# Optimization experiments

Hardware: AMD Instinct MI355X
Metric: run time of the kernel (lower is better)

## Reference

```python
import jax, jax.numpy as jnp
import numpy as np

NUM_ENT = 100000
NUM_REL = 500            # distinct relations; table holds 2*NUM_REL (forward + inverse)
E = 500000               # total edges: first half original, second half reversed
D = 200                  # init_dim = gcn_dim = embed_dim
B = 256
KW, KH = 10, 20          # ConvE reshape: 2*KW*KH == 2*D
NF, KS = 200, 7
FLAT = (2 * KW - KS + 1) * (KH - KS + 1) * NF  # 14*14*200 = 39200
EPS = 1e-5


def setup_inputs() -> dict:
    key = jax.random.key(0)
    k = jax.random.split(key, 24)
    half = E // 2
    src = jax.random.randint(k[0], (half,), 0, NUM_ENT)
    dst = jax.random.randint(k[1], (half,), 0, NUM_ENT)
    et = jax.random.randint(k[2], (half,), 0, NUM_REL)
    edge_index = jnp.stack([jnp.concatenate([src, dst]), jnp.concatenate([dst, src])])
    edge_type = jnp.concatenate([et, et + NUM_REL])
    sub = jax.random.randint(k[3], (B,), 0, NUM_ENT)
    rel = jax.random.randint(k[4], (B,), 0, 2 * NUM_REL)
    g = lambda i, shape, s=0.05: jax.random.normal(k[i], shape, jnp.float32) * s
    return dict(
        sub=sub, rel=rel, edge_index=edge_index, edge_type=edge_type,
        init_embed=g(5, (NUM_ENT, D)), init_rel=g(6, (2 * NUM_REL, D)),
        loop_rel1=g(7, (1, D)), loop_rel2=g(8, (1, D)),
        w_in1=g(9, (D, D)), w_out1=g(10, (D, D)), w_loop1=g(11, (D, D)), w_rel1=g(12, (D, D)), b1=jnp.zeros((D,), jnp.float32),
        w_in2=g(13, (D, D)), w_out2=g(14, (D, D)), w_loop2=g(15, (D, D)), w_rel2=g(16, (D, D)), b2=jnp.zeros((D,), jnp.float32),
        conv_w=g(17, (NF, 1, KS, KS)), conv_b=jnp.zeros((NF,), jnp.float32),
        bn0_g=jnp.ones((1,), jnp.float32), bn0_b=jnp.zeros((1,), jnp.float32),
        bn1_g=jnp.ones((NF,), jnp.float32), bn1_b=jnp.zeros((NF,), jnp.float32),
        bn2_g=jnp.ones((D,), jnp.float32), bn2_b=jnp.zeros((D,), jnp.float32),
        fc_w=g(18, (FLAT, D)), fc_b=jnp.zeros((D,), jnp.float32),
        ent_bias=jnp.zeros((NUM_ENT,), jnp.float32),
    )


def _bn2d(x, g, b):  # eval-mode BN: running mean 0, running var 1
    s = g / jnp.sqrt(1.0 + EPS)
    return x * s[None, :, None, None] + b[None, :, None, None]


def _bn1d(x, g, b):
    return x * (g / jnp.sqrt(1.0 + EPS)) + b


def _agg(x_src, rel_e, dst, w):
    # message = comp(h_src, h_rel) @ W   (subtraction composition), degree-normalized scatter
    m = (x_src - rel_e) @ w                                        # [E/2, D]
    s = jax.ops.segment_sum(m, dst, num_segments=NUM_ENT)          # [N, D]
    deg = jax.ops.segment_sum(jnp.ones(dst.shape, m.dtype), dst, num_segments=NUM_ENT)
    return s / jnp.clip(deg, 1.0)[:, None]


def _ragcn_layer(x, r, ei, et, w_in, w_out, w_loop, w_rel, loop_rel, b):
    half = ei.shape[1] // 2
    src, dst = ei[0], ei[1]
    re = r[et]                                                     # [E, D]
    res = (_agg(x[src[:half]], re[:half], dst[:half], w_in)
           + _agg(x[src[half:]], re[half:], dst[half:], w_out)
           + (x - loop_rel) @ w_loop)
    return jnp.tanh(res / 3.0 + b), r @ w_rel


def _forward(sub, rel, edge_index, edge_type, init_embed, init_rel,
             loop_rel1, loop_rel2, w_in1, w_out1, w_loop1, w_rel1, b1,
             w_in2, w_out2, w_loop2, w_rel2, b2, conv_w, conv_b,
             bn0_g, bn0_b, bn1_g, bn1_b, bn2_g, bn2_b, fc_w, fc_b, ent_bias):
    x, r = _ragcn_layer(init_embed, init_rel, edge_index, edge_type, w_in1, w_out1, w_loop1, w_rel1, loop_rel1, b1)
    x, r = _ragcn_layer(x, r, edge_index, edge_type, w_in2, w_out2, w_loop2, w_rel2, loop_rel2, b2)
    sub_emb = x[sub]                                               # [B, D]
    rel_emb = r[rel]                                               # [B, D]
    # ConvE concat: [B,2,D] -> [B,D,2] -> [B,1,2*KW,KH]
    stk = jnp.transpose(jnp.stack([sub_emb, rel_emb], axis=1), (0, 2, 1)).reshape(-1, 1, 2 * KW, KH)
    h = _bn2d(stk, bn0_g, bn0_b)
    h = jax.lax.conv_general_dilated(h, conv_w, (1, 1), 'VALID',
                                     dimension_numbers=('NCHW', 'OIHW', 'NCHW'))
    h = h + conv_b[None, :, None, None]
    h = jax.nn.relu(_bn2d(h, bn1_g, bn1_b))
    h = h.reshape(-1, FLAT)
    h = h @ fc_w + fc_b
    h = jax.nn.relu(_bn1d(h, bn2_g, bn2_b))
    logits = h @ x.T + ent_bias                                    # [B, NUM_ENT]
    return jax.nn.sigmoid(logits)


def reference(sub, rel, edge_index, edge_type, init_embed, init_rel,
              loop_rel1, loop_rel2, w_in1, w_out1, w_loop1, w_rel1, b1,
              w_in2, w_out2, w_loop2, w_rel2, b2, conv_w, conv_b,
              bn0_g, bn0_b, bn1_g, bn1_b, bn2_g, bn2_b, fc_w, fc_b, ent_bias):
    return _forward(sub, rel, edge_index, edge_type, init_embed, init_rel,
                    loop_rel1, loop_rel2, w_in1, w_out1, w_loop1, w_rel1, b1,
                    w_in2, w_out2, w_loop2, w_rel2, b2, conv_w, conv_b,
                    bn0_g, bn0_b, bn1_g, bn1_b, bn2_g, bn2_b, fc_w, fc_b, ent_bias)
```

## Files before the change

kernel.cpp:

```cpp
#include <hip/hip_runtime.h>
#include <math.h>

#define N_ENT   100000
#define N_REL2  1000
#define E_TOT   500000
#define E_HALF  250000
#define DIM     200
#define BB      256
#define NFILT   200
#define FLATK   39200
#define EPS_BN  1e-5f

#define NROWS   200000
#define SCHUNK  2048
#define SNBLK   ((NROWS + SCHUNK - 1) / SCHUNK)

#define FC_KC   175
#define FC_KLEN 224

typedef __attribute__((ext_vector_type(8))) short bf16x8;
typedef __attribute__((ext_vector_type(4))) float f32x4;

__device__ __forceinline__ unsigned short f2b(float f) {
    union { float f; unsigned u; } c; c.f = f;
    unsigned u = c.u;
    u += 0x7fffu + ((u >> 16) & 1u);
    return (unsigned short)(u >> 16);
}
__device__ __forceinline__ float b2f(unsigned short h) {
    union { unsigned u; float f; } c; c.u = ((unsigned)h) << 16;
    return c.f;
}
__device__ __forceinline__ float fast_tanh(float x) {
    float ax = fabsf(x);
    float e = __expf(-2.0f * ax);
    float t = (1.0f - e) / (1.0f + e);
    return copysignf(t, x);
}

__global__ void convert_kernel(const float* __restrict__ s, unsigned short* __restrict__ d,
                               int n) {
    int i = (blockIdx.x * 256 + threadIdx.x) * 4;
    if (i + 3 < n) {
        float4 v = *(const float4*)(s + i);
        ushort4 o;
        o.x = f2b(v.x); o.y = f2b(v.y); o.z = f2b(v.z); o.w = f2b(v.w);
        *(ushort4*)(d + i) = o;
    } else {
        for (; i < n; ++i) d[i] = f2b(s[i]);
    }
}

__global__ void wstack_kernel(const float* __restrict__ wIn, const float* __restrict__ wOut,
                              const float* __restrict__ wLoop, unsigned short* __restrict__ WTK) {
    int g = blockIdx.x * 256 + threadIdx.x;
    if (g >= 3 * 28 * 224 * 8) return;
    int kk = g & 7;
    int t = g >> 3;
    int col = t % 224;
    int t2 = t / 224;
    int unit = t2 % 28;
    int seg = t2 / 28;
    int k = unit * 8 + kk;
    float v = 0.f;
    if (col < 200 && k < 200)
        v = (seg == 0 ? wIn : seg == 1 ? wOut : wLoop)[k * 200 + col];
    WTK[g] = f2b(v);
}

__global__ void fwt_kernel(const float* __restrict__ fw, unsigned short* __restrict__ FWT) {
    __shared__ float t[32][33];
    const int bid = blockIdx.x;
    const int kt = bid % 1225, jt = bid / 1225;
    const int tid = threadIdx.x;
#pragma unroll
    for (int it = 0; it < 4; ++it) {
        int idx = tid + it * 256;
        int kk = idx >> 5, jj = idx & 31;
        int j = jt * 32 + jj;
        t[kk][jj] = (j < 200) ? fw[(size_t)(kt * 32 + kk) * 200 + j] : 0.f;
    }
    __syncthreads();
#pragma unroll
    for (int it = 0; it < 4; ++it) {
        int idx = tid + it * 256;
        int jj = idx >> 5, kk = idx & 31;
        int j = jt * 32 + jj;
        if (j < 208)
            FWT[(size_t)j * FLATK + kt * 32 + kk] = f2b(t[kk][jj]);
    }
}

__global__ void hist_kernel(const int* __restrict__ ei, int* __restrict__ cnt) {
    int e = blockIdx.x * 256 + threadIdx.x;
    if (e >= E_TOT) return;
    int row = ei[E_TOT + e] + (e < E_HALF ? 0 : N_ENT);
    atomicAdd(&cnt[row], 1);
}

__global__ void scan1_kernel(const int* __restrict__ cnt, int* __restrict__ row_start,
                             int* __restrict__ blockSum) {
    __shared__ int tsum[256];
    const int t = threadIdx.x;
    const int base = blockIdx.x * SCHUNK + t * 8;
    int v[8];
    int s = 0;
#pragma unroll
    for (int i = 0; i < 8; ++i) {
        int idx = base + i;
        int c = (idx < NROWS) ? cnt[idx] : 0;
        v[i] = s;
        s += c;
    }
    tsum[t] = s;
    __syncthreads();
    for (int off = 1; off < 256; off <<= 1) {
        int x = (t >= off) ? tsum[t - off] : 0;
        __syncthreads();
        if (t >= off) tsum[t] += x;
        __syncthreads();
    }
    int texc = (t == 0) ? 0 : tsum[t - 1];
    if (t == 0) blockSum[blockIdx.x] = tsum[255];
#pragma unroll
    for (int i = 0; i < 8; ++i) {
        int idx = base + i;
        if (idx < NROWS) row_start[idx] = texc + v[i];
    }
}

__global__ void scan2_kernel(int* __restrict__ blockSum) {
    int s = 0;
    for (int i = 0; i < SNBLK; ++i) { int c = blockSum[i]; blockSum[i] = s; s += c; }
}

__global__ void scan3_kernel(int* __restrict__ row_start, int* __restrict__ row_cur,
                             const int* __restrict__ blockSum) {
    int i = blockIdx.x * 256 + threadIdx.x;
    if (i >= NROWS) return;
    int v = row_start[i] + blockSum[i / SCHUNK];
    row_start[i] = v;
    row_cur[i] = v;
}

__global__ void fill_kernel(const int* __restrict__ ei, const int* __restrict__ et,
                            int* __restrict__ row_cur, int2* __restrict__ epair) {
    int e = blockIdx.x * 256 + threadIdx.x;
    if (e >= E_TOT) return;
    int row = ei[E_TOT + e] + (e < E_HALF ? 0 : N_ENT);
    int pos = atomicAdd(&row_cur[row], 1);
    epair[pos] = make_int2(ei[e], et[e]);
}

__global__ void gather_kernel(const unsigned short* __restrict__ x,
                              const unsigned short* __restrict__ r,
                              const int2* __restrict__ epair,
                              const int* __restrict__ row_start, const int* __restrict__ cnt,
                              unsigned short* __restrict__ agg) {
    int wid = blockIdx.x * 4 + (threadIdx.x >> 6);
    if (wid >= NROWS) return;
    int lane = threadIdx.x & 63;
    if (lane >= 50) return;
    int start = row_start[wid];
    int deg = cnt[wid];
    float a0 = 0.f, a1 = 0.f, a2 = 0.f, a3 = 0.f;
    float c0 = 0.f, c1 = 0.f, c2 = 0.f, c3 = 0.f;
    int i = 0;
    for (; i + 2 <= deg; i += 2) {
        int2 e0 = epair[start + i];
        int2 e1 = epair[start + i + 1];
        ushort4 xv0 = *(const ushort4*)(x + (size_t)e0.x * DIM + lane * 4);
        ushort4 rv0 = *(const ushort4*)(r + (size_t)e0.y * DIM + lane * 4);
        ushort4 xv1 = *(const ushort4*)(x + (size_t)e1.x * DIM + lane * 4);
        ushort4 rv1 = *(const ushort4*)(r + (size_t)e1.y * DIM + lane * 4);
        a0 += b2f(xv0.x) - b2f(rv0.x);
        a1 += b2f(xv0.y) - b2f(rv0.y);
        a2 += b2f(xv0.z) - b2f(rv0.z);
        a3 += b2f(xv0.w) - b2f(rv0.w);
        c0 += b2f(xv1.x) - b2f(rv1.x);
        c1 += b2f(xv1.y) - b2f(rv1.y);
        c2 += b2f(xv1.z) - b2f(rv1.z);
        c3 += b2f(xv1.w) - b2f(rv1.w);
    }
    if (i < deg) {
        int2 e = epair[start + i];
        ushort4 xv = *(const ushort4*)(x + (size_t)e.x * DIM + lane * 4);
        ushort4 rv = *(const ushort4*)(r + (size_t)e.y * DIM + lane * 4);
        a0 += b2f(xv.x) - b2f(rv.x);
        a1 += b2f(xv.y) - b2f(rv.y);
        a2 += b2f(xv.z) - b2f(rv.z);
        a3 += b2f(xv.w) - b2f(rv.w);
    }
    float sc = 1.0f / fmaxf((float)deg, 1.0f);
    ushort4 o;
    o.x = f2b((a0 + c0) * sc);
    o.y = f2b((a1 + c1) * sc);
    o.z = f2b((a2 + c2) * sc);
    o.w = f2b((a3 + c3) * sc);
    *(ushort4*)(agg + (size_t)wid * DIM + lane * 4) = o;
}

__global__ void lv_kernel(const float* __restrict__ lr, const float* __restrict__ wl,
                          float* __restrict__ lv) {
    int j = blockIdx.x * blockDim.x + threadIdx.x;
    if (j >= DIM) return;
    float acc = 0.f;
    for (int k = 0; k < DIM; ++k) acc += lr[k] * wl[k * DIM + j];
    lv[j] = acc;
}

__global__ void rgemm_kernel(const float* __restrict__ r, const float* __restrict__ w,
                             float* __restrict__ out, int rows) {
    int g = blockIdx.x * 256 + threadIdx.x;
    if (g >= rows * DIM) return;
    int i = g / DIM, j = g - i * DIM;
    float acc = 0.f;
    for (int k = 0; k < DIM; ++k) acc += r[i * DIM + k] * w[k * DIM + j];
    out[g] = acc;
}

#define LOAD_A1(g, slot) do {                                                   \
    const unsigned short* Ap_ = Aseg[(g) / 7];                                  \
    apf[slot] = *(const bf16x8*)(Ap_ + (size_t)arow * 200 + ((g) % 7) * 32 + lq * 8); \
} while (0)

__global__ __launch_bounds__(256, 5) void layer_mfma_kernel(
        const unsigned short* __restrict__ aggI, const unsigned short* __restrict__ aggO,
        const unsigned short* __restrict__ xin, const unsigned short* __restrict__ WTK,
        const float* __restrict__ lv, const float* __restrict__ bias,
        unsigned short* __restrict__ out, int nwg) {
    __shared__ unsigned short Wl[16 * 112 * 8];
    const int bid = blockIdx.x;
    const int q = nwg >> 3, rr = nwg & 7;
    const int xcd = bid & 7, idx = bid >> 3;
    const int L = (xcd < rr ? xcd * (q + 1) : rr * (q + 1) + (xcd - rr) * q) + idx;
    const int rowblk  = L >> 1;
    const int colbase = (L & 1) * 112;

    const int tid  = threadIdx.x;
    const int wm   = tid >> 6;
    const int lane = tid & 63;
    const int lr   = lane & 15;
    const int lq   = lane >> 4;
    const int row0 = rowblk * 64;
    const int arow = row0 + wm * 16 + lr;

    const unsigned short* const Aseg[3] = { aggI, aggO, xin };

    f32x4 acc[7];
#pragma unroll
    for (int n = 0; n < 7; ++n) acc[n] = (f32x4){0.f, 0.f, 0.f, 0.f};

    bf16x8 apf[4];
    LOAD_A1(0, 0);
    LOAD_A1(1, 1);
    LOAD_A1(2, 2);

#pragma unroll
    for (int seg = 0; seg < 3; ++seg) {
#pragma unroll
        for (int ph = 0; ph < 2; ++ph) {
            if (seg + ph) __syncthreads();
            if (ph == 0) {
#pragma unroll
                for (int it = 0; it < 7; ++it) {
                    int u = tid + it * 256;
                    int unit = u >> 7 , col;
                    unit = u / 112; col = u - unit * 112;
                    *(int4*)(&Wl[(unit * 112 + col) * 8]) =
                        *(const int4*)(WTK + ((size_t)(seg * 28 + unit) * 224 + colbase + col) * 8);
                }
            } else {
                for (int u = tid; u < 1344; u += 256) {
                    int unit = u / 112, col = u - unit * 112;
                    *(int4*)(&Wl[(unit * 112 + col) * 8]) =
                        *(const int4*)(WTK + ((size_t)(seg * 28 + 16 + unit) * 224 + colbase + col) * 8);
                }
            }
            __syncthreads();
            const int NC = (ph == 0) ? 4 : 3;
#pragma unroll
            for (int cc = 0; cc < NC; ++cc) {
                const int g = seg * 7 + (ph ? 4 : 0) + cc;
                if (g + 3 < 21) LOAD_A1(g + 3, (g + 3) & 3);
                __builtin_amdgcn_s_setprio(1);
#pragma unroll
                for (int n = 0; n < 7; ++n) {
                    bf16x8 b = *(const bf16x8*)(&Wl[((cc * 4 + lq) * 112 + n * 16 + lr) * 8]);
                    acc[n] = __builtin_amdgcn_mfma_f32_16x16x32_bf16(apf[g & 3], b, acc[n], 0, 0, 0);
                }
                __builtin_amdgcn_s_setprio(0);
            }
        }
    }

    {
        int rbase = row0 + wm * 16 + lq * 4;
#pragma unroll
        for (int n = 0; n < 7; ++n) {
            int col = colbase + n * 16 + lr;
            if (col < 200) {
                float lvc = lv[col], bc = bias[col];
#pragma unroll
                for (int r2 = 0; r2 < 4; ++r2) {
                    int row = rbase + r2;
                    if (row < N_ENT) {
                        float v = (acc[n][r2] - lvc) * (1.0f / 3.0f) + bc;
                        out[(size_t)row * 200 + col] = f2b(fast_tanh(v));
                    }
                }
            }
        }
    }
}

__global__ void img_kernel(const unsigned short* __restrict__ x, const float* __restrict__ r,
                           const int* __restrict__ sub, const int* __restrict__ rel,
                           const float* __restrict__ bn0g, const float* __restrict__ bn0b,
                           unsigned short* __restrict__ img) {
    int g = blockIdx.x * 256 + threadIdx.x;
    if (g >= BB * 2 * DIM) return;
    int b = g / 400, l = g - b * 400;
    int d = l >> 1;
    float v = (l & 1) ? r[(size_t)rel[b] * DIM + d] : b2f(x[(size_t)sub[b] * DIM + d]);
    float s0 = bn0g[0] * rsqrtf(1.0f + EPS_BN);
    img[g] = f2b(v * s0 + bn0b[0]);
}

__global__ void im2col_kernel(const unsigned short* __restrict__ img,
                              unsigned short* __restrict__ IM) {
    int g = blockIdx.x * 256 + threadIdx.x;
    if (g >= 50176 * 64) return;
    int row = g >> 6, k = g & 63;
    int b = row / 196, p = row - b * 196;
    int h = p / 14, w = p - h * 14;
    unsigned short v = 0;
    if (k < 49) {
        int i = k / 7, j = k - i * 7;
        v = img[b * 400 + (h + i) * 20 + (w + j)];
    }
    IM[g] = v;
}

__global__ void cwt_kernel(const float* __restrict__ cw, unsigned short* __restrict__ CWT) {
    int g = blockIdx.x * 256 + threadIdx.x;
    if (g >= 208 * 64) return;
    int f = g >> 6, k = g & 63;
    CWT[g] = (f < 200 && k < 49) ? f2b(cw[f * 49 + k]) : 0;
}

__global__ __launch_bounds__(256) void conv_mfma_kernel(
        const unsigned short* __restrict__ IM, const unsigned short* __restrict__ CWT,
        const float* __restrict__ cb, const float* __restrict__ bn1g,
        const float* __restrict__ bn1b, unsigned short* __restrict__ CO_B) {
    const int tid  = threadIdx.x;
    const int row0 = blockIdx.x * 128;
    const int wave = tid >> 6;
    const int lane = tid & 63;
    const int lr   = lane & 15;
    const int lq   = lane >> 4;
    const int arow = row0 + wave * 32 + lr;

    f32x4 acc[2][13];
#pragma unroll
    for (int m = 0; m < 2; ++m)
#pragma unroll
        for (int n = 0; n < 13; ++n) acc[m][n] = (f32x4){0.f, 0.f, 0.f, 0.f};

#pragma unroll
    for (int c = 0; c < 2; ++c) {
        const int k = c * 32 + lq * 8;
        bf16x8 a0 = *(const bf16x8*)(IM + (size_t)arow * 64 + k);
        bf16x8 a1 = *(const bf16x8*)(IM + (size_t)(arow + 16) * 64 + k);
#pragma unroll
        for (int n = 0; n < 13; ++n) {
            bf16x8 b = *(const bf16x8*)(CWT + (size_t)(n * 16 + lr) * 64 + k);
            acc[0][n] = __builtin_amdgcn_mfma_f32_16x16x32_bf16(a0, b, acc[0][n], 0, 0, 0);
            acc[1][n] = __builtin_amdgcn_mfma_f32_16x16x32_bf16(a1, b, acc[1][n], 0, 0, 0);
        }
    }

#pragma unroll
    for (int m = 0; m < 2; ++m) {
        int grow_base = row0 + wave * 32 + m * 16 + lq * 4;
#pragma unroll
        for (int n = 0; n < 13; ++n) {
            int col = n * 16 + lr;
            if (col < 200) {
                float s1 = bn1g[col] * rsqrtf(1.0f + EPS_BN);
                float t1 = bn1b[col];
                float cbf = cb[col];
#pragma unroll
                for (int r = 0; r < 4; ++r) {
                    int grow = grow_base + r;
                    int b = grow / 196, p = grow - b * 196;
                    float v = fmaxf((acc[m][n][r] + cbf) * s1 + t1, 0.f);
                    CO_B[(size_t)b * FLATK + col * 196 + p] = f2b(v);
                }
            }
        }
    }
}

__global__ __launch_bounds__(256) void fc_mfma_kernel(
        const unsigned short* __restrict__ CO_B, const unsigned short* __restrict__ FWT,
        float* __restrict__ partials) {
    const int tid  = threadIdx.x;
    const int kc   = blockIdx.x >> 2;
    const int mb   = blockIdx.x & 3;
    const int wave = tid >> 6;
    const int lane = tid & 63;
    const int lr   = lane & 15;
    const int lq   = lane >> 4;
    const int m0   = mb * 64 + wave * 16;

    f32x4 acc[13];
#pragma unroll
    for (int n = 0; n < 13; ++n) acc[n] = (f32x4){0.f, 0.f, 0.f, 0.f};

#pragma unroll
    for (int s = 0; s < 7; ++s) {
        const int k = kc * FC_KLEN + s * 32 + lq * 8;
        bf16x8 a = *(const bf16x8*)(CO_B + (size_t)(m0 + lr) * FLATK + k);
#pragma unroll
        for (int n = 0; n < 13; ++n) {
            bf16x8 b = *(const bf16x8*)(FWT + (size_t)(n * 16 + lr) * FLATK + k);
            acc[n] = __builtin_amdgcn_mfma_f32_16x16x32_bf16(a, b, acc[n], 0, 0, 0);
        }
    }

    float* slab = partials + (size_t)kc * (BB * 208);
#pragma unroll
    for (int n = 0; n < 13; ++n) {
        int col = n * 16 + lr;
#pragma unroll
        for (int r = 0; r < 4; ++r) {
            int row = m0 + lq * 4 + r;
            slab[(size_t)row * 208 + col] = acc[n][r];
        }
    }
}

__global__ void fc_reduce_kernel(const float* __restrict__ partials,
                                 const float* __restrict__ fcb,
                                 const float* __restrict__ g2, const float* __restrict__ b2v,
                                 unsigned short* __restrict__ hb) {
    int g = blockIdx.x * 256 + threadIdx.x;
    if (g >= BB * 224) return;
    int b = g / 224, j = g - b * 224;
    unsigned short o = 0;
    if (j < 200) {
        float s = 0.f;
        const float* p = partials + (size_t)b * 208 + j;
#pragma unroll 5
        for (int c = 0; c < FC_KC; ++c)
            s += p[(size_t)c * (BB * 208)];
        float v = (s + fcb[j]) * (g2[j] * rsqrtf(1.0f + EPS_BN)) + b2v[j];
        o = f2b(fmaxf(v, 0.f));
    }
    hb[g] = o;
}

#define LOAD_HB(g, buf) do {                                                    \
    const unsigned short* base_ = hb + (size_t)brow * 224 + (g) * 32 + lq * 8;  \
    buf[0] = *(const bf16x8*)(base_);                                           \
    buf[1] = *(const bf16x8*)(base_ + 16 * 224);                                \
} while (0)

__global__ __launch_bounds__(512, 2) void logits_mfma_kernel(
        const unsigned short* __restrict__ x, const unsigned short* __restrict__ hb,
        const float* __restrict__ eb, float* __restrict__ out, int nwg) {
    __shared__ unsigned short Xl[112 * 136];
    const int bid = blockIdx.x;
    const int q = nwg >> 3, rr = nwg & 7;
    const int xcd = bid & 7, idx = bid >> 3;
    const int nb = (xcd < rr ? xcd * (q + 1) : rr * (q + 1) + (xcd - rr) * q) + idx;
    const int ent0 = nb * 112;

    const int tid  = threadIdx.x;
    const int wave = tid >> 6;
    const int mh   = wave >> 2;
    const int wm   = wave & 3;
    const int lane = tid & 63;
    const int lr   = lane & 15;
    const int lq   = lane >> 4;
    const int brow = mh * 128 + wm * 32 + lr;

    f32x4 acc[2][7];
#pragma unroll
    for (int m = 0; m < 2; ++m)
#pragma unroll
        for (int n = 0; n < 7; ++n) acc[m][n] = (f32x4){0.f, 0.f, 0.f, 0.f};

    bf16x8 apf[3][2];
    LOAD_HB(0, apf[0]);
    LOAD_HB(1, apf[1]);

#pragma unroll
    for (int ph = 0; ph < 2; ++ph) {
        if (ph) __syncthreads();
        if (ph == 0) {
#pragma unroll
            for (int it = 0; it < 4; ++it) {
                int u = tid + it * 512;
                if (u < 1792) {
                    int row = u >> 4, c = u & 15;
                    int ent = ent0 + row;
                    int4 v = make_int4(0, 0, 0, 0);
                    if (ent < N_ENT)
                        v = *(const int4*)(x + (size_t)ent * 200 + c * 8);
                    *(int4*)(&Xl[row * 136 + c * 8]) = v;
                }
            }
        } else {
            for (int u = tid; u < 1344; u += 512) {
                int row = u / 12, c = u - row * 12;
                int gu = 16 + c;
                int ent = ent0 + row;
                int4 v = make_int4(0, 0, 0, 0);
                if (ent < N_ENT && gu < 25)
                    v = *(const int4*)(x + (size_t)ent * 200 + gu * 8);
                *(int4*)(&Xl[row * 136 + c * 8]) = v;
            }
        }
        __syncthreads();
        const int NC = (ph == 0) ? 4 : 3;
#pragma unroll
        for (int cc = 0; cc < NC; ++cc) {
            const int g = (ph ? 4 : 0) + cc;
            if (g + 2 < 7) LOAD_HB(g + 2, apf[(g + 2) % 3]);
#pragma unroll
            for (int n = 0; n < 7; ++n) {
                bf16x8 b = *(const bf16x8*)(&Xl[(n * 16 + lr) * 136 + cc * 32 + lq * 8]);
                acc[0][n] = __builtin_amdgcn_mfma_f32_16x16x32_bf16(apf[g % 3][0], b, acc[0][n], 0, 0, 0);
                acc[1][n] = __builtin_amdgcn_mfma_f32_16x16x32_bf16(apf[g % 3][1], b, acc[1][n], 0, 0, 0);
            }
        }
    }

#pragma unroll
    for (int m = 0; m < 2; ++m) {
        int b_base = mh * 128 + wm * 32 + m * 16 + lq * 4;
#pragma unroll
        for (int n = 0; n < 7; ++n) {
            int ent = ent0 + n * 16 + lr;
            if (ent < N_ENT) {
                float bias = eb[ent];
#pragma unroll
                for (int r = 0; r < 4; ++r) {
                    float v = acc[m][n][r] + bias;
                    out[(size_t)(b_base + r) * N_ENT + ent] = 1.0f / (1.0f + __expf(-v));
                }
            }
        }
    }
}

extern "C" void kernel_launch(void* const* d_in, const int* in_sizes, int n_in,
                              void* d_out, int out_size, void* d_ws, size_t ws_size,
                              hipStream_t stream) {
    const int*   sub        = (const int*)  d_in[0];
    const int*   rel        = (const int*)  d_in[1];
    const int*   edge_index = (const int*)  d_in[2];
    const int*   edge_type  = (const int*)  d_in[3];
    const float* init_embed = (const float*)d_in[4];
    const float* init_rel   = (const float*)d_in[5];
    const float* loop_rel1  = (const float*)d_in[6];
    const float* loop_rel2  = (const float*)d_in[7];
    const float* w_in1      = (const float*)d_in[8];
    const float* w_out1     = (const float*)d_in[9];
    const float* w_loop1    = (const float*)d_in[10];
    const float* w_rel1     = (const float*)d_in[11];
    const float* b1         = (const float*)d_in[12];
    const float* w_in2      = (const float*)d_in[13];
    const float* w_out2     = (const float*)d_in[14];
    const float* w_loop2    = (const float*)d_in[15];
    const float* w_rel2     = (const float*)d_in[16];
    const float* b2         = (const float*)d_in[17];
    const float* conv_w     = (const float*)d_in[18];
    const float* conv_b     = (const float*)d_in[19];
    const float* bn0_g      = (const float*)d_in[20];
    const float* bn0_b      = (const float*)d_in[21];
    const float* bn1_g      = (const float*)d_in[22];
    const float* bn1_b      = (const float*)d_in[23];
    const float* bn2_g      = (const float*)d_in[24];
    const float* bn2_b      = (const float*)d_in[25];
    const float* fc_w       = (const float*)d_in[26];
    const float* fc_b       = (const float*)d_in[27];
    const float* ent_bias   = (const float*)d_in[28];

    unsigned short* aggb = (unsigned short*)d_ws;
    unsigned short* x0b  = aggb + 40000000;
    unsigned short* x1b  = x0b  + 20000000;
    unsigned short* r0b  = x1b  + 20000000;
    unsigned short* r1b  = r0b  + 200000;
    unsigned short* WTK  = r1b  + 200000;
    unsigned short* img  = WTK  + 150528;
    unsigned short* IM   = img  + 102400;
    unsigned short* CWT  = IM   + 3211264;
    unsigned short* CO_B = CWT  + 13312;
    unsigned short* hb16 = CO_B + 10035200;
    unsigned short* FWT  = hb16 + 57344;
    float* fbase = (float*)(FWT + 8153600);
    float* r1f      = fbase;
    float* r2f      = r1f  + 200000;
    float* lv       = r2f  + 200000;
    float* partials = lv   + 256;

    int2* epair    = (int2*)CO_B;
    int* cnt       = (int*)(epair + E_TOT);
    int* row_start = cnt  + NROWS;
    int* row_cur   = row_start + NROWS;
    int* blockSum  = row_cur + NROWS;

    unsigned short* aggIb = aggb;
    unsigned short* aggOb = aggb + (size_t)N_ENT * DIM;
    unsigned short* x2b   = x0b;

    const int gather_blocks = (NROWS + 3) / 4;
    const int layer_nwg     = ((N_ENT + 63) / 64) * 2;
    const int logits_nwg    = (N_ENT + 111) / 112;
    const int wstack_blocks = (3 * 28 * 224 * 8 + 255) / 256;

    convert_kernel<<<(N_ENT * DIM + 1023) / 1024, 256, 0, stream>>>(init_embed, x0b, N_ENT * DIM);
    convert_kernel<<<(N_REL2 * DIM + 1023) / 1024, 256, 0, stream>>>(init_rel, r0b, N_REL2 * DIM);
    hipMemsetAsync(cnt, 0, (size_t)NROWS * 4, stream);
    hist_kernel<<<(E_TOT + 255) / 256, 256, 0, stream>>>(edge_index, cnt);
    scan1_kernel<<<SNBLK, 256, 0, stream>>>(cnt, row_start, blockSum);
    scan2_kernel<<<1, 1, 0, stream>>>(blockSum);
    scan3_kernel<<<(NROWS + 255) / 256, 256, 0, stream>>>(row_start, row_cur, blockSum);
    fill_kernel<<<(E_TOT + 255) / 256, 256, 0, stream>>>(edge_index, edge_type, row_cur, epair);

    wstack_kernel<<<wstack_blocks, 256, 0, stream>>>(w_in1, w_out1, w_loop1, WTK);
    gather_kernel<<<gather_blocks, 256, 0, stream>>>(x0b, r0b, epair, row_start, cnt, aggb);
    lv_kernel<<<1, 256, 0, stream>>>(loop_rel1, w_loop1, lv);
    layer_mfma_kernel<<<layer_nwg, 256, 0, stream>>>(aggIb, aggOb, x0b, WTK, lv, b1, x1b, layer_nwg);
    rgemm_kernel<<<(N_REL2 * DIM + 255) / 256, 256, 0, stream>>>(init_rel, w_rel1, r1f, N_REL2);
    convert_kernel<<<(N_REL2 * DIM + 1023) / 1024, 256, 0, stream>>>(r1f, r1b, N_REL2 * DIM);

    wstack_kernel<<<wstack_blocks, 256, 0, stream>>>(w_in2, w_out2, w_loop2, WTK);
    gather_kernel<<<gather_blocks, 256, 0, stream>>>(x1b, r1b, epair, row_start, cnt, aggb);
    lv_kernel<<<1, 256, 0, stream>>>(loop_rel2, w_loop2, lv);
    layer_mfma_kernel<<<layer_nwg, 256, 0, stream>>>(aggIb, aggOb, x1b, WTK, lv, b2, x2b, layer_nwg);
    rgemm_kernel<<<(N_REL2 * DIM + 255) / 256, 256, 0, stream>>>(r1f, w_rel2, r2f, N_REL2);

    img_kernel<<<(BB * 400 + 255) / 256, 256, 0, stream>>>(x2b, r2f, sub, rel,
                                                           bn0_g, bn0_b, img);
    im2col_kernel<<<(50176 * 64 + 255) / 256, 256, 0, stream>>>(img, IM);
    cwt_kernel<<<(208 * 64 + 255) / 256, 256, 0, stream>>>(conv_w, CWT);
    conv_mfma_kernel<<<50176 / 128, 256, 0, stream>>>(IM, CWT, conv_b, bn1_g, bn1_b, CO_B);
    fwt_kernel<<<1225 * 7, 256, 0, stream>>>(fc_w, FWT);
    fc_mfma_kernel<<<FC_KC * 4, 256, 0, stream>>>(CO_B, FWT, partials);
    fc_reduce_kernel<<<(BB * 224 + 255) / 256, 256, 0, stream>>>(partials, fc_b, bn2_g, bn2_b, hb16);

    logits_mfma_kernel<<<logits_nwg, 512, 0, stream>>>(x2b, hb16, ent_bias, (float*)d_out,
                                                       logits_nwg);
}
```

Baseline: 588.2 us.

## Double-buffer weight tiles in LDS with register prefetch in layer GEMM

Replaces the six-phase load-sync-compute loop for weight tiles with a double-buffered LDS scheme. Each stage holds two k-chunks, and the next stage is fetched into registers while MFMAs run on the current buffer. This is meant to hide global-load latency of the weight tiles behind compute and reduce exposed barrier stalls. In exchange there are more barriers (eleven stages), extra registers for staging, and launch bounds drop from 5 to 4 blocks per SM, which lowers occupancy.

```diff
diff --git a/kernel.cpp b/kernel.cpp
--- a/kernel.cpp
+++ b/kernel.cpp
@@ -224,12 +224,38 @@
     apf[slot] = *(const bf16x8*)(Ap_ + (size_t)arow * 200 + ((g) % 7) * 32 + lq * 8); \
 } while (0)
 
-__global__ __launch_bounds__(256, 5) void layer_mfma_kernel(
+#define STAGE_LOAD(s) do {                                                       \
+    _Pragma("unroll")                                                            \
+    for (int it = 0; it < 4; ++it) {                                             \
+        int u = tid + it * 256;                                                  \
+        if (u < 896) {                                                           \
+            int slot = u / 448;                                                  \
+            int rem  = u - slot * 448;                                           \
+            int ui   = rem / 112, col = rem - ui * 112;                          \
+            int g2   = (s) * 2 + slot;                                           \
+            if (g2 < 21) {                                                       \
+                int sg = g2 / 7, kc = g2 % 7;                                    \
+                vals[it] = *(const int4*)(WTK +                                  \
+                    ((size_t)(sg * 28 + kc * 4 + ui) * 224 + colbase + col) * 8);\
+            } else vals[it] = make_int4(0, 0, 0, 0);                             \
+        }                                                                        \
+    }                                                                            \
+} while (0)
+
+#define STAGE_WRITE(b) do {                                                      \
+    _Pragma("unroll")                                                            \
+    for (int it = 0; it < 4; ++it) {                                             \
+        int u = tid + it * 256;                                                  \
+        if (u < 896) *(int4*)(&Wl[(b)][u * 8]) = vals[it];                       \
+    }                                                                            \
+} while (0)
+
+__global__ __launch_bounds__(256, 4) void layer_mfma_kernel(
         const unsigned short* __restrict__ aggI, const unsigned short* __restrict__ aggO,
         const unsigned short* __restrict__ xin, const unsigned short* __restrict__ WTK,
         const float* __restrict__ lv, const float* __restrict__ bias,
         unsigned short* __restrict__ out, int nwg) {
-    __shared__ unsigned short Wl[16 * 112 * 8];
+    __shared__ unsigned short Wl[2][8 * 112 * 8];
     const int bid = blockIdx.x;
     const int q = nwg >> 3, rr = nwg & 7;
     const int xcd = bid & 7, idx = bid >> 3;
@@ -256,42 +282,30 @@
     LOAD_A1(1, 1);
     LOAD_A1(2, 2);
 
-#pragma unroll
-    for (int seg = 0; seg < 3; ++seg) {
-#pragma unroll
-        for (int ph = 0; ph < 2; ++ph) {
-            if (seg + ph) __syncthreads();
-            if (ph == 0) {
-#pragma unroll
-                for (int it = 0; it < 7; ++it) {
-                    int u = tid + it * 256;
-                    int unit = u >> 7 , col;
-                    unit = u / 112; col = u - unit * 112;
-                    *(int4*)(&Wl[(unit * 112 + col) * 8]) =
-                        *(const int4*)(WTK + ((size_t)(seg * 28 + unit) * 224 + colbase + col) * 8);
-                }
-            } else {
-                for (int u = tid; u < 1344; u += 256) {
-                    int unit = u / 112, col = u - unit * 112;
-                    *(int4*)(&Wl[(unit * 112 + col) * 8]) =
-                        *(const int4*)(WTK + ((size_t)(seg * 28 + 16 + unit) * 224 + colbase + col) * 8);
-                }
+    int4 vals[4];
+
+    STAGE_LOAD(0);
+    STAGE_WRITE(0);
+    __syncthreads();
+
+#pragma unroll
+    for (int p = 0; p < 11; ++p) {
+        if (p < 10) STAGE_LOAD(p + 1);
+        const int NC = (p < 10) ? 2 : 1;
+#pragma unroll
+        for (int cc = 0; cc < NC; ++cc) {
+            const int g = p * 2 + cc;
+            if (g + 3 < 21) LOAD_A1(g + 3, (g + 3) & 3);
+            __builtin_amdgcn_s_setprio(1);
+#pragma unroll
+            for (int n = 0; n < 7; ++n) {
+                bf16x8 b = *(const bf16x8*)(&Wl[p & 1][((cc * 4 + lq) * 112 + n * 16 + lr) * 8]);
+                acc[n] = __builtin_amdgcn_mfma_f32_16x16x32_bf16(apf[g & 3], b, acc[n], 0, 0, 0);
             }
-            __syncthreads();
-            const int NC = (ph == 0) ? 4 : 3;
-#pragma unroll
-            for (int cc = 0; cc < NC; ++cc) {
-                const int g = seg * 7 + (ph ? 4 : 0) + cc;
-                if (g + 3 < 21) LOAD_A1(g + 3, (g + 3) & 3);
-                __builtin_amdgcn_s_setprio(1);
-#pragma unroll
-                for (int n = 0; n < 7; ++n) {
-                    bf16x8 b = *(const bf16x8*)(&Wl[((cc * 4 + lq) * 112 + n * 16 + lr) * 8]);
-                    acc[n] = __builtin_amdgcn_mfma_f32_16x16x32_bf16(apf[g & 3], b, acc[n], 0, 0, 0);
-                }
-                __builtin_amdgcn_s_setprio(0);
-            }
-        }
+            __builtin_amdgcn_s_setprio(0);
+        }
+        if (p < 10) STAGE_WRITE((p + 1) & 1);
+        __syncthreads();
     }
 
     {
```

Result: faster. 569.2 us (median of 2 runs) (-3.2%).

## Switch layer GEMM to 32x32x16 MFMA with 128-row full-width tiles and double-buffered weights

Applied to the files above, without the earlier changes.

Reworks the per-layer MFMA kernel so each workgroup covers 128 rows and all 224 output columns, not 64 rows by half the columns. It uses 32x32x16 bf16 MFMA instructions and double-buffers the weight slices in LDS, prefetching the next stage into registers during compute. This removes duplicate A-row loads across the two column halves and overlaps weight staging with math. The cost is more accumulator registers and lower occupancy (launch bounds drop from 5 to 3 waves per SIMD), plus fewer workgroups overall.

```diff
diff --git a/kernel.cpp b/kernel.cpp
--- a/kernel.cpp
+++ b/kernel.cpp
@@ -20,6 +20,7 @@
 
 typedef __attribute__((ext_vector_type(8))) short bf16x8;
 typedef __attribute__((ext_vector_type(4))) float f32x4;
+typedef __attribute__((ext_vector_type(16))) float f32x16;
 
 __device__ __forceinline__ unsigned short f2b(float f) {
     union { float f; unsigned u; } c; c.f = f;
@@ -219,93 +220,99 @@
     out[g] = acc;
 }
 
-#define LOAD_A1(g, slot) do {                                                   \
-    const unsigned short* Ap_ = Aseg[(g) / 7];                                  \
-    apf[slot] = *(const bf16x8*)(Ap_ + (size_t)arow * 200 + ((g) % 7) * 32 + lq * 8); \
+#define LOAD_A32(g, slot) do {                                                   \
+    const unsigned short* Ap_ = Aseg[(g) / 14];                                   \
+    apf[slot] = *(const bf16x8*)(Ap_ + (size_t)arow * 200 + ((g) % 14) * 16 + kh8);\
 } while (0)
 
-__global__ __launch_bounds__(256, 5) void layer_mfma_kernel(
+#define STAGE_LOAD32(s) do {                                                      \
+    _Pragma("unroll")                                                             \
+    for (int it = 0; it < 4; ++it) {                                              \
+        int u = tid + it * 256;                                                   \
+        if (u < 896) {                                                            \
+            int ui = u / 224, col = u - ui * 224;                                 \
+            vals[it] = *(const int4*)(WTK + ((size_t)(4 * (s) + ui) * 224 + col) * 8); \
+        }                                                                         \
+    }                                                                             \
+} while (0)
+
+#define STAGE_WRITE32(b) do {                                                     \
+    _Pragma("unroll")                                                             \
+    for (int it = 0; it < 4; ++it) {                                              \
+        int u = tid + it * 256;                                                   \
+        if (u < 896) *(int4*)(&Wl[(b)][u * 8]) = vals[it];                        \
+    }                                                                             \
+} while (0)
+
+__global__ __launch_bounds__(256, 3) void layer_mfma_kernel(
         const unsigned short* __restrict__ aggI, const unsigned short* __restrict__ aggO,
         const unsigned short* __restrict__ xin, const unsigned short* __restrict__ WTK,
         const float* __restrict__ lv, const float* __restrict__ bias,
         unsigned short* __restrict__ out, int nwg) {
-    __shared__ unsigned short Wl[16 * 112 * 8];
+    __shared__ unsigned short Wl[2][4 * 224 * 8];
     const int bid = blockIdx.x;
     const int q = nwg >> 3, rr = nwg & 7;
     const int xcd = bid & 7, idx = bid >> 3;
     const int L = (xcd < rr ? xcd * (q + 1) : rr * (q + 1) + (xcd - rr) * q) + idx;
-    const int rowblk  = L >> 1;
-    const int colbase = (L & 1) * 112;
-
-    const int tid  = threadIdx.x;
-    const int wm   = tid >> 6;
-    const int lane = tid & 63;
-    const int lr   = lane & 15;
-    const int lq   = lane >> 4;
-    const int row0 = rowblk * 64;
-    const int arow = row0 + wm * 16 + lr;
+
+    const int tid   = threadIdx.x;
+    const int wm    = tid >> 6;
+    const int lane  = tid & 63;
+    const int ln31  = lane & 31;
+    const int khalf = lane >> 5;
+    const int kh8   = khalf * 8;
+    const int row0  = L * 128;
+    const int arow  = row0 + wm * 32 + ln31;
 
     const unsigned short* const Aseg[3] = { aggI, aggO, xin };
 
-    f32x4 acc[7];
-#pragma unroll
-    for (int n = 0; n < 7; ++n) acc[n] = (f32x4){0.f, 0.f, 0.f, 0.f};
+    f32x16 acc[7];
+#pragma unroll
+    for (int n = 0; n < 7; ++n)
+#pragma unroll
+        for (int r = 0; r < 16; ++r) acc[n][r] = 0.f;
 
     bf16x8 apf[4];
-    LOAD_A1(0, 0);
-    LOAD_A1(1, 1);
-    LOAD_A1(2, 2);
-
-#pragma unroll
-    for (int seg = 0; seg < 3; ++seg) {
-#pragma unroll
-        for (int ph = 0; ph < 2; ++ph) {
-            if (seg + ph) __syncthreads();
-            if (ph == 0) {
-#pragma unroll
-                for (int it = 0; it < 7; ++it) {
-                    int u = tid + it * 256;
-                    int unit = u >> 7 , col;
-                    unit = u / 112; col = u - unit * 112;
-                    *(int4*)(&Wl[(unit * 112 + col) * 8]) =
-                        *(const int4*)(WTK + ((size_t)(seg * 28 + unit) * 224 + colbase + col) * 8);
-                }
-            } else {
-                for (int u = tid; u < 1344; u += 256) {
-                    int unit = u / 112, col = u - unit * 112;
-                    *(int4*)(&Wl[(unit * 112 + col) * 8]) =
-                        *(const int4*)(WTK + ((size_t)(seg * 28 + 16 + unit) * 224 + colbase + col) * 8);
-                }
+    LOAD_A32(0, 0);
+    LOAD_A32(1, 1);
+    LOAD_A32(2, 2);
+
+    int4 vals[4];
+
+    STAGE_LOAD32(0);
+    STAGE_WRITE32(0);
+    __syncthreads();
+
+#pragma unroll
+    for (int p = 0; p < 21; ++p) {
+        if (p < 20) STAGE_LOAD32(p + 1);
+#pragma unroll
+        for (int cc = 0; cc < 2; ++cc) {
+            const int g = p * 2 + cc;
+            if (g + 3 < 42) LOAD_A32(g + 3, (g + 3) & 3);
+            __builtin_amdgcn_s_setprio(1);
+#pragma unroll
+            for (int n = 0; n < 7; ++n) {
+                bf16x8 b = *(const bf16x8*)(&Wl[p & 1][((cc * 2 + khalf) * 224 + n * 32 + ln31) * 8]);
+                acc[n] = __builtin_amdgcn_mfma_f32_32x32x16_bf16(apf[g & 3], b, acc[n], 0, 0, 0);
             }
-            __syncthreads();
-            const int NC = (ph == 0) ? 4 : 3;
-#pragma unroll
-            for (int cc = 0; cc < NC; ++cc) {
-                const int g = seg * 7 + (ph ? 4 : 0) + cc;
-                if (g + 3 < 21) LOAD_A1(g + 3, (g + 3) & 3);
-                __builtin_amdgcn_s_setprio(1);
-#pragma unroll
-                for (int n = 0; n < 7; ++n) {
-                    bf16x8 b = *(const bf16x8*)(&Wl[((cc * 4 + lq) * 112 + n * 16 + lr) * 8]);
-                    acc[n] = __builtin_amdgcn_mfma_f32_16x16x32_bf16(apf[g & 3], b, acc[n], 0, 0, 0);
-                }
-                __builtin_amdgcn_s_setprio(0);
-            }
-        }
+            __builtin_amdgcn_s_setprio(0);
+        }
+        if (p < 20) STAGE_WRITE32((p + 1) & 1);
+        __syncthreads();
     }
 
     {
-        int rbase = row0 + wm * 16 + lq * 4;
 #pragma unroll
         for (int n = 0; n < 7; ++n) {
-            int col = colbase + n * 16 + lr;
+            int col = n * 32 + ln31;
             if (col < 200) {
                 float lvc = lv[col], bc = bias[col];
 #pragma unroll
-                for (int r2 = 0; r2 < 4; ++r2) {
-                    int row = rbase + r2;
+                for (int r = 0; r < 16; ++r) {
+                    int row = row0 + wm * 32 + (r & 3) + 8 * (r >> 2) + 4 * khalf;
                     if (row < N_ENT) {
-                        float v = (acc[n][r2] - lvc) * (1.0f / 3.0f) + bc;
+                        float v = (acc[n][r] - lvc) * (1.0f / 3.0f) + bc;
                         out[(size_t)row * 200 + col] = f2b(fast_tanh(v));
                     }
                 }
@@ -618,7 +625,7 @@
     unsigned short* x2b   = x0b;
 
     const int gather_blocks = (NROWS + 3) / 4;
-    const int layer_nwg     = ((N_ENT + 63) / 64) * 2;
+    const int layer_nwg     = (N_ENT + 127) / 128;
     const int logits_nwg    = (N_ENT + 111) / 112;
     const int wstack_blocks = (3 * 28 * 224 * 8 + 255) / 256;
 
```

Result: slower. 830.3 us (+41.2%).
